# Kernel optimization log

Measured on AMD Instinct MI355X. Metric: run time of the kernel, lower is better.

The kernel has to match this reference:

```python
import jax, jax.numpy as jnp
import numpy as np

MU = 1.0          # stability parameter
DT = 0.01         # Euler step
EPS = 1e-9        # matches E in the torch source
BOUND = float(np.pi / 2)  # hard_bounds = (-pi/2, pi/2)
N_NODES = 200_000
N_EDGES = 12_800_000  # avg degree 64


def setup_inputs() -> dict:
    key = jax.random.key(0)
    ks = jax.random.split(key, 9)
    n, ne = N_NODES, N_EDGES
    # distributions mirror the torch initialization
    x = jax.random.normal(ks[0], (n,), jnp.float32) * 0.1
    y = jax.random.normal(ks[1], (n,), jnp.float32) * 0.1
    w = (jax.random.uniform(ks[2], (n,), jnp.float32) * 2 - 1) * 4.0 + 2.0
    amplitudes = (jax.random.uniform(ks[3], (n,), jnp.float32) * 2 - 1) * 2.0 + 1.0
    phase = (jax.random.uniform(ks[4], (n,), jnp.float32) * 2 - 1) * np.pi
    ha = jax.random.normal(ks[5], (n,), jnp.float32) * 0.5
    b = jax.random.normal(ks[6], (n,), jnp.float32) * 0.1
    edge_src = jax.random.randint(ks[7], (ne,), 0, n, jnp.int32)
    edge_dst = jax.random.randint(ks[8], (ne,), 0, n, jnp.int32)
    return {"x": x, "y": y, "w": w, "amplitudes": amplitudes, "phase": phase,
            "ha": ha, "b": b, "edge_src": edge_src, "edge_dst": edge_dst}


def reference(x, y, w, amplitudes, phase, ha, b, edge_src, edge_dst):
    n = x.shape[0]
    # r^2 = x^2 + y^2 + E  (torch computes sqrt(..+E) then squares it)
    r2 = x * x + y * y + EPS
    dx = (MU - r2) * x - w * y
    dy = (MU - r2) * y + w * x
    # edge coupling: for edge (j=src -> i=dst):
    #   d*_i += ha_i * sin(theta_j - theta_i) * (*_j - *_i)
    theta = jnp.arctan2(y, x + EPS)                       # [n]
    coef = ha[edge_dst] * jnp.sin(theta[edge_src] - theta[edge_dst])  # [ne]
    cx = jax.ops.segment_sum(coef * (x[edge_src] - x[edge_dst]), edge_dst, num_segments=n)
    cy = jax.ops.segment_sum(coef * (y[edge_src] - y[edge_dst]), edge_dst, num_segments=n)
    # Euler step (x update is internal state; angles depend only on new y)
    y_new = y + (dy + cy) * DT
    x_new = x + (dx + cx) * DT
    angles = amplitudes * y_new + phase + b
    angles = jnp.clip(angles, -BOUND, BOUND)
    return angles
```

## Files before the change

### kernel.cpp

```cpp
#include <hip/hip_runtime.h>
#include <hip/hip_bf16.h>

#define MU_V    1.0f
#define DT_V    0.01f
#define EPS_V   1e-9f
#define BOUND_V 1.5707963267948966f

constexpr int NPB     = 1024;
constexpr int LOG_NPB = 10;
constexpr int NB_MAX  = 256;
constexpr int B1      = 512;
constexpr int EPT     = 16;
constexpr int EPB     = B1 * EPT;
constexpr int CAP     = 68608;
constexpr int RB      = 256;

static_assert(NB_MAX == 256, "block scan below assumes NB_MAX == 256 (4 waves)");

typedef unsigned uint4v __attribute__((ext_vector_type(4)));

__global__ void node_pre_kernel(const float* __restrict__ x_,
                                const float* __restrict__ y_,
                                const float* __restrict__ ha_,
                                float4* __restrict__ pack,
                                unsigned* __restrict__ zbuf,
                                int n, int nz) {
    int i = blockIdx.x * blockDim.x + threadIdx.x;
    if (i < nz) zbuf[i] = 0u;
    if (i >= n) return;
    float x = x_[i];
    float y = y_[i];
    float xe = x + EPS_V;
    float r2 = xe * xe + y * y;
    float s, c;
    if (r2 > 0.0f) {
        float rinv = rsqrtf(r2);
        s = y * rinv;
        c = xe * rinv;
    } else {
        s = 0.0f;
        c = 1.0f;
    }
    pack[i] = make_float4(s, c, y, ha_[i]);
}

__global__ __launch_bounds__(B1)
void bucket_scatter_kernel(const int* __restrict__ src,
                           const int* __restrict__ dst,
                           unsigned* __restrict__ cursors,
                           unsigned* __restrict__ buf,
                           int ne, int nb) {
    __shared__ unsigned cnt[NB_MAX];
    __shared__ unsigned gbase[NB_MAX];
    __shared__ unsigned lofs[NB_MAX];
    __shared__ unsigned loc[NB_MAX];
    __shared__ unsigned wsum[4];
    __shared__ unsigned ents[EPB];

    int tid = threadIdx.x;
    for (int i = tid; i < NB_MAX; i += B1) cnt[i] = 0u;
    __syncthreads();
    long long base = (long long)blockIdx.x * EPB;

    if (base + EPB <= ne) {
        int4 rs4[EPT / 4], rd4[EPT / 4];
        #pragma unroll
        for (int it = 0; it < EPT / 4; ++it) {
            long long e = base + ((long long)(it * B1 + tid)) * 4;
            rs4[it] = *(const int4*)(src + e);
            rd4[it] = *(const int4*)(dst + e);
        }
        const int* sv = (const int*)rs4;
        const int* dv = (const int*)rd4;
        #pragma unroll
        for (int k = 0; k < EPT; ++k)
            atomicAdd(&cnt[((unsigned)dv[k]) >> LOG_NPB], 1u);
        __syncthreads();

        unsigned myc = 0u, incl = 0u;
        if (tid < NB_MAX) {
            myc = cnt[tid];
            incl = myc;
            #pragma unroll
            for (int d = 1; d < 64; d <<= 1) {
                unsigned up = __shfl_up(incl, d);
                if ((tid & 63) >= d) incl += up;
            }
            if ((tid & 63) == 63) wsum[tid >> 6] = incl;
        }
        __syncthreads();
        if (tid < NB_MAX) {
            unsigned wp = 0u;
            int w = tid >> 6;
            #pragma unroll
            for (int k = 0; k < 3; ++k)
                if (k < w) wp += wsum[k];
            lofs[tid] = wp + incl - myc;
            gbase[tid] = myc ? atomicAdd(&cursors[tid], myc) : 0u;
            loc[tid] = 0u;
        }
        __syncthreads();

        #pragma unroll
        for (int k = 0; k < EPT; ++k) {
            unsigned d = (unsigned)dv[k];
            unsigned s = (unsigned)sv[k];
            unsigned b = d >> LOG_NPB;
            unsigned p = atomicAdd(&loc[b], 1u);
            ents[lofs[b] + p] = (s << LOG_NPB) | (d & (NPB - 1));
        }
        __syncthreads();

        int wave = tid >> 6;
        int lane = tid & 63;
        for (int b = wave; b < nb; b += (B1 / 64)) {
            unsigned c  = cnt[b];
            unsigned gb = gbase[b];
            unsigned lo = lofs[b];
            for (unsigned i = (unsigned)lane; i < c; i += 64u) {
                unsigned p = gb + i;
                if (p < (unsigned)CAP)
                    buf[(size_t)b * CAP + p] = ents[lo + i];
            }
        }
    } else {
        #pragma unroll
        for (int it = 0; it < EPT / 4; ++it) {
            long long e = base + ((long long)(it * B1 + tid)) * 4;
            if (e + 4 <= ne) {
                int4 d4 = *(const int4*)(dst + e);
                atomicAdd(&cnt[((unsigned)d4.x) >> LOG_NPB], 1u);
                atomicAdd(&cnt[((unsigned)d4.y) >> LOG_NPB], 1u);
                atomicAdd(&cnt[((unsigned)d4.z) >> LOG_NPB], 1u);
                atomicAdd(&cnt[((unsigned)d4.w) >> LOG_NPB], 1u);
            } else if (e < ne) {
                for (long long q = e; q < ne; ++q)
                    atomicAdd(&cnt[((unsigned)dst[q]) >> LOG_NPB], 1u);
            }
        }
        __syncthreads();
        for (int b = tid; b < nb; b += B1) {
            unsigned c = cnt[b];
            gbase[b] = c ? atomicAdd(&cursors[b], c) : 0u;
            loc[b] = 0u;
        }
        __syncthreads();
        #pragma unroll
        for (int it = 0; it < EPT / 4; ++it) {
            long long e = base + ((long long)(it * B1 + tid)) * 4;
            if (e + 4 <= ne) {
                int4 s4 = *(const int4*)(src + e);
                int4 d4 = *(const int4*)(dst + e);
                {
                    unsigned d = (unsigned)d4.x, s = (unsigned)s4.x, b = d >> LOG_NPB;
                    unsigned pos = gbase[b] + atomicAdd(&loc[b], 1u);
                    if (pos < (unsigned)CAP) buf[(size_t)b * CAP + pos] = (s << LOG_NPB) | (d & (NPB - 1));
                }
                {
                    unsigned d = (unsigned)d4.y, s = (unsigned)s4.y, b = d >> LOG_NPB;
                    unsigned pos = gbase[b] + atomicAdd(&loc[b], 1u);
                    if (pos < (unsigned)CAP) buf[(size_t)b * CAP + pos] = (s << LOG_NPB) | (d & (NPB - 1));
                }
                {
                    unsigned d = (unsigned)d4.z, s = (unsigned)s4.z, b = d >> LOG_NPB;
                    unsigned pos = gbase[b] + atomicAdd(&loc[b], 1u);
                    if (pos < (unsigned)CAP) buf[(size_t)b * CAP + pos] = (s << LOG_NPB) | (d & (NPB - 1));
                }
                {
                    unsigned d = (unsigned)d4.w, s = (unsigned)s4.w, b = d >> LOG_NPB;
                    unsigned pos = gbase[b] + atomicAdd(&loc[b], 1u);
                    if (pos < (unsigned)CAP) buf[(size_t)b * CAP + pos] = (s << LOG_NPB) | (d & (NPB - 1));
                }
            } else if (e < ne) {
                for (long long q = e; q < ne; ++q) {
                    unsigned d = (unsigned)dst[q], s = (unsigned)src[q], b = d >> LOG_NPB;
                    unsigned pos = gbase[b] + atomicAdd(&loc[b], 1u);
                    if (pos < (unsigned)CAP) buf[(size_t)b * CAP + pos] = (s << LOG_NPB) | (d & (NPB - 1));
                }
            }
        }
    }
}

__device__ __forceinline__ void reduce_entry(unsigned ent,
                                             const float4* __restrict__ pack,
                                             const float4* __restrict__ plocal,
                                             float* __restrict__ acc) {
    unsigned s  = ent >> LOG_NPB;
    unsigned dl = ent & (NPB - 1);
    float4 ps = pack[s];
    float4 pd = plocal[dl];
    float v = (pd.w * (ps.x * pd.y - ps.y * pd.x)) * (ps.z - pd.z);
    atomicAdd(&acc[dl], v);
}

__device__ __forceinline__ void reduce_proc(unsigned ent, float4 ps,
                                            const float4* __restrict__ plocal,
                                            float* __restrict__ acc) {
    unsigned dl = ent & (NPB - 1);
    float4 pd = plocal[dl];
    float v = (pd.w * (ps.x * pd.y - ps.y * pd.x)) * (ps.z - pd.z);
    atomicAdd(&acc[dl], v);
}

__global__ __launch_bounds__(RB)
void bucket_reduce_kernel(const unsigned* __restrict__ cursors,
                          const unsigned* __restrict__ buf,
                          const float4* __restrict__ pack,
                          float* __restrict__ partial, int n, int nsub) {
    __shared__ float4 plocal[NPB];
    __shared__ float  acc[NPB];
    int b   = blockIdx.x / nsub;
    int sub = blockIdx.x % nsub;
    int tid = threadIdx.x;
    int node0 = b << LOG_NPB;
    for (int k = tid; k < NPB; k += RB) {
        int d = node0 + k;
        plocal[k] = (d < n) ? pack[d] : make_float4(0.f, 0.f, 0.f, 0.f);
        acc[k] = 0.0f;
    }
    __syncthreads();
    unsigned count = cursors[b];
    if (count > (unsigned)CAP) count = (unsigned)CAP;
    unsigned chunk = (((count + nsub - 1) / nsub) + 7u) & ~7u;
    unsigned lo = (unsigned)sub * chunk;
    unsigned hi = lo + chunk;
    if (hi > count) hi = count;
    unsigned span = (hi > lo) ? (hi - lo) : 0u;
    unsigned vend = lo + (span & ~7u);
    const unsigned* mybuf = buf + (size_t)b * CAP;

    unsigned i = lo + (unsigned)tid * 8u;
    if (i < vend) {
        uint4v a4 = __builtin_nontemporal_load((const uint4v*)(mybuf + i));
        uint4v b4 = __builtin_nontemporal_load((const uint4v*)(mybuf + i + 4));
        while (true) {
            float4 g0 = pack[a4.x >> LOG_NPB];
            float4 g1 = pack[a4.y >> LOG_NPB];
            float4 g2 = pack[a4.z >> LOG_NPB];
            float4 g3 = pack[a4.w >> LOG_NPB];
            float4 g4 = pack[b4.x >> LOG_NPB];
            float4 g5 = pack[b4.y >> LOG_NPB];
            float4 g6 = pack[b4.z >> LOG_NPB];
            float4 g7 = pack[b4.w >> LOG_NPB];
            unsigned ni = i + (unsigned)RB * 8u;
            bool more = ni < vend;
            uint4v na4 = a4, nb4 = b4;
            if (more) {
                na4 = __builtin_nontemporal_load((const uint4v*)(mybuf + ni));
                nb4 = __builtin_nontemporal_load((const uint4v*)(mybuf + ni + 4));
            }
            reduce_proc(a4.x, g0, plocal, acc);
            reduce_proc(a4.y, g1, plocal, acc);
            reduce_proc(a4.z, g2, plocal, acc);
            reduce_proc(a4.w, g3, plocal, acc);
            reduce_proc(b4.x, g4, plocal, acc);
            reduce_proc(b4.y, g5, plocal, acc);
            reduce_proc(b4.z, g6, plocal, acc);
            reduce_proc(b4.w, g7, plocal, acc);
            if (!more) break;
            i = ni; a4 = na4; b4 = nb4;
        }
    }
    {
        unsigned idx = vend + (unsigned)tid;
        if (idx < hi)
            reduce_entry(mybuf[idx], pack, plocal, acc);
    }
    __syncthreads();
    float* myp = partial + ((size_t)b * nsub + sub) * NPB;
    for (int k = tid; k < NPB; k += RB)
        __builtin_nontemporal_store(acc[k], &myp[k]);
}

__device__ __forceinline__ void edge_one(int s, int d,
                                         const float4* __restrict__ pack,
                                         float* __restrict__ cy) {
    float4 ps = pack[s];
    float4 pd = pack[d];
    float v = (pd.w * (ps.x * pd.y - ps.y * pd.x)) * (ps.z - pd.z);
    atomicAdd(&cy[d], v);
}

__global__ void edge_kernel(const int* __restrict__ src,
                            const int* __restrict__ dst,
                            const float4* __restrict__ pack,
                            float* __restrict__ cy, int ne) {
    int t = blockIdx.x * blockDim.x + threadIdx.x;
    long long base = (long long)t * 4;
    if (base >= ne) return;
    if (base + 4 <= ne) {
        int4 s4 = *(const int4*)(src + base);
        int4 d4 = *(const int4*)(dst + base);
        edge_one(s4.x, d4.x, pack, cy);
        edge_one(s4.y, d4.y, pack, cy);
        edge_one(s4.z, d4.z, pack, cy);
        edge_one(s4.w, d4.w, pack, cy);
    } else {
        for (long long e = base; e < ne; ++e)
            edge_one(src[e], dst[e], pack, cy);
    }
}

__global__ void finalize_fast_kernel(const float* __restrict__ x_,
                                     const float* __restrict__ y_,
                                     const float* __restrict__ w_,
                                     const float* __restrict__ amp_,
                                     const float* __restrict__ ph_,
                                     const float* __restrict__ b_,
                                     const float* __restrict__ partial,
                                     float* __restrict__ out, int n, int nsub) {
    int i = blockIdx.x * blockDim.x + threadIdx.x;
    if (i >= n) return;
    int bk = i >> LOG_NPB;
    int dl = i & (NPB - 1);
    float cy = 0.0f;
    for (int s = 0; s < nsub; ++s)
        cy += partial[((size_t)bk * nsub + s) * NPB + dl];
    float x = x_[i];
    float y = y_[i];
    float w = w_[i];
    float r2 = x * x + y * y + EPS_V;
    float dy = (MU_V - r2) * y + w * x;
    float y_new = y + (dy + cy) * DT_V;
    float ang = amp_[i] * y_new + ph_[i] + b_[i];
    ang = fminf(fmaxf(ang, -BOUND_V), BOUND_V);
    out[i] = ang;
}

__global__ void finalize_kernel(const float* __restrict__ x_,
                                const float* __restrict__ y_,
                                const float* __restrict__ w_,
                                const float* __restrict__ amp_,
                                const float* __restrict__ ph_,
                                const float* __restrict__ b_,
                                const float* __restrict__ cy,
                                float* __restrict__ out, int n) {
    int i = blockIdx.x * blockDim.x + threadIdx.x;
    if (i >= n) return;
    float x = x_[i];
    float y = y_[i];
    float w = w_[i];
    float r2 = x * x + y * y + EPS_V;
    float dy = (MU_V - r2) * y + w * x;
    float y_new = y + (dy + cy[i]) * DT_V;
    float ang = amp_[i] * y_new + ph_[i] + b_[i];
    ang = fminf(fmaxf(ang, -BOUND_V), BOUND_V);
    out[i] = ang;
}

extern "C" void kernel_launch(void* const* d_in, const int* in_sizes, int n_in,
                              void* d_out, int out_size, void* d_ws, size_t ws_size,
                              hipStream_t stream) {
    const float* x_   = (const float*)d_in[0];
    const float* y_   = (const float*)d_in[1];
    const float* w_   = (const float*)d_in[2];
    const float* amp_ = (const float*)d_in[3];
    const float* ph_  = (const float*)d_in[4];
    const float* ha_  = (const float*)d_in[5];
    const float* b_   = (const float*)d_in[6];
    const int* edge_src = (const int*)d_in[7];
    const int* edge_dst = (const int*)d_in[8];
    float* out = (float*)d_out;

    int n  = in_sizes[0];
    int ne = in_sizes[7];
    int nb = (n + NPB - 1) >> LOG_NPB;

    auto align256 = [](size_t v) { return (v + 255) & ~(size_t)255; };
    size_t off_pack    = 0;
    size_t off_cursors = align256(off_pack + (size_t)n * 16);
    size_t off_partial = align256(off_cursors + (size_t)nb * 4);

    int nsub = 0;
    size_t off_buf = 0;
    for (int cand : {16, 12, 8, 4, 2, 1}) {
        size_t ob = align256(off_partial + (size_t)nb * cand * NPB * 4);
        if (ob + (size_t)nb * CAP * 4 <= ws_size) { nsub = cand; off_buf = ob; break; }
    }

    float4*   pack    = (float4*)((char*)d_ws + off_pack);
    unsigned* cursors = (unsigned*)((char*)d_ws + off_cursors);
    float*    cy      = (float*)((char*)d_ws + off_cursors);
    float*    partial = (float*)((char*)d_ws + off_partial);
    unsigned* buf     = (unsigned*)((char*)d_ws + off_buf);

    bool fast = (nsub > 0) && (nb <= NB_MAX) &&
                ((long long)n <= (1LL << (31 - LOG_NPB)));

    const int B = 256;
    if (fast) {
        node_pre_kernel<<<(n + B - 1) / B, B, 0, stream>>>(
            x_, y_, ha_, pack, cursors, n, nb);
        int blocks1 = (ne + EPB - 1) / EPB;
        bucket_scatter_kernel<<<blocks1, B1, 0, stream>>>(
            edge_src, edge_dst, cursors, buf, ne, nb);
        bucket_reduce_kernel<<<nb * nsub, RB, 0, stream>>>(
            cursors, buf, pack, partial, n, nsub);
        finalize_fast_kernel<<<(n + B - 1) / B, B, 0, stream>>>(
            x_, y_, w_, amp_, ph_, b_, partial, out, n, nsub);
    } else {
        node_pre_kernel<<<(n + B - 1) / B, B, 0, stream>>>(
            x_, y_, ha_, pack, (unsigned*)cy, n, n);
        int ngroups = (ne + 3) / 4;
        edge_kernel<<<(ngroups + B - 1) / B, B, 0, stream>>>(
            edge_src, edge_dst, pack, cy, ne);
        finalize_kernel<<<(n + B - 1) / B, B, 0, stream>>>(
            x_, y_, w_, amp_, ph_, b_, cy, out, n);
    }
}
```

Baseline: 261.7 us.

## Fuse node precompute into scatter and finalize into reduce via last-block ticket

Folds the node trig/pack precompute into the bucket scatter kernel and the final Euler/clip step into the bucket reduce kernel. The last sub-block per bucket is picked with an atomic ticket and threadfence, so four launches become two plus a memset. It also narrows the scatter write-out groups from 64 to 16 lanes and drops the software-pipelined prefetch in the reduce loop. The aim is to cut launch and small-kernel overhead, at the cost of extra fence/atomic work and possibly less latency hiding in the reduce loop.

```diff
diff --git a/kernel.cpp b/kernel.cpp
--- a/kernel.cpp
+++ b/kernel.cpp
@@ -16,6 +16,7 @@
 constexpr int RB      = 256;
 
 static_assert(NB_MAX == 256, "block scan below assumes NB_MAX == 256 (4 waves)");
+static_assert((CAP & 7) == 0, "CAP must be a multiple of 8 for vectored reads");
 
 typedef unsigned uint4v __attribute__((ext_vector_type(4)));
 
@@ -45,11 +46,15 @@
 }
 
 __global__ __launch_bounds__(B1)
-void bucket_scatter_kernel(const int* __restrict__ src,
+void bucket_scatter_kernel(const float* __restrict__ x_,
+                           const float* __restrict__ y_,
+                           const float* __restrict__ ha_,
+                           float4* __restrict__ pack,
+                           const int* __restrict__ src,
                            const int* __restrict__ dst,
                            unsigned* __restrict__ cursors,
                            unsigned* __restrict__ buf,
-                           int ne, int nb) {
+                           int ne, int nb, int n) {
     __shared__ unsigned cnt[NB_MAX];
     __shared__ unsigned gbase[NB_MAX];
     __shared__ unsigned lofs[NB_MAX];
@@ -58,6 +63,29 @@
     __shared__ unsigned ents[EPB];
 
     int tid = threadIdx.x;
+
+    {
+        int ns = (n + (int)gridDim.x - 1) / (int)gridDim.x;
+        int i0 = (int)blockIdx.x * ns;
+        int i1 = i0 + ns; if (i1 > n) i1 = n;
+        for (int i = i0 + tid; i < i1; i += B1) {
+            float x = x_[i];
+            float y = y_[i];
+            float xe = x + EPS_V;
+            float r2 = xe * xe + y * y;
+            float s, c;
+            if (r2 > 0.0f) {
+                float rinv = rsqrtf(r2);
+                s = y * rinv;
+                c = xe * rinv;
+            } else {
+                s = 0.0f;
+                c = 1.0f;
+            }
+            pack[i] = make_float4(s, c, y, ha_[i]);
+        }
+    }
+
     for (int i = tid; i < NB_MAX; i += B1) cnt[i] = 0u;
     __syncthreads();
     long long base = (long long)blockIdx.x * EPB;
@@ -111,13 +139,13 @@
         }
         __syncthreads();
 
-        int wave = tid >> 6;
-        int lane = tid & 63;
-        for (int b = wave; b < nb; b += (B1 / 64)) {
+        int grp = tid >> 4;
+        int l16 = tid & 15;
+        for (int b = grp; b < nb; b += (B1 / 16)) {
             unsigned c  = cnt[b];
             unsigned gb = gbase[b];
             unsigned lo = lofs[b];
-            for (unsigned i = (unsigned)lane; i < c; i += 64u) {
+            for (unsigned i = (unsigned)l16; i < c; i += 16u) {
                 unsigned p = gb + i;
                 if (p < (unsigned)CAP)
                     buf[(size_t)b * CAP + p] = ents[lo + i];
@@ -204,12 +232,22 @@
 }
 
 __global__ __launch_bounds__(RB)
-void bucket_reduce_kernel(const unsigned* __restrict__ cursors,
-                          const unsigned* __restrict__ buf,
-                          const float4* __restrict__ pack,
-                          float* __restrict__ partial, int n, int nsub) {
+void bucket_reduce_fin_kernel(const unsigned* __restrict__ cursors,
+                              unsigned* __restrict__ done,
+                              const unsigned* __restrict__ buf,
+                              const float4* __restrict__ pack,
+                              float* __restrict__ partial,
+                              const float* __restrict__ x_,
+                              const float* __restrict__ y_,
+                              const float* __restrict__ w_,
+                              const float* __restrict__ amp_,
+                              const float* __restrict__ ph_,
+                              const float* __restrict__ b_,
+                              float* __restrict__ out,
+                              int n, int nsub) {
     __shared__ float4 plocal[NPB];
     __shared__ float  acc[NPB];
+    __shared__ unsigned ticket_s;
     int b   = blockIdx.x / nsub;
     int sub = blockIdx.x % nsub;
     int tid = threadIdx.x;
@@ -230,37 +268,25 @@
     unsigned vend = lo + (span & ~7u);
     const unsigned* mybuf = buf + (size_t)b * CAP;
 
-    unsigned i = lo + (unsigned)tid * 8u;
-    if (i < vend) {
+    for (unsigned i = lo + (unsigned)tid * 8u; i < vend; i += (unsigned)RB * 8u) {
         uint4v a4 = __builtin_nontemporal_load((const uint4v*)(mybuf + i));
         uint4v b4 = __builtin_nontemporal_load((const uint4v*)(mybuf + i + 4));
-        while (true) {
-            float4 g0 = pack[a4.x >> LOG_NPB];
-            float4 g1 = pack[a4.y >> LOG_NPB];
-            float4 g2 = pack[a4.z >> LOG_NPB];
-            float4 g3 = pack[a4.w >> LOG_NPB];
-            float4 g4 = pack[b4.x >> LOG_NPB];
-            float4 g5 = pack[b4.y >> LOG_NPB];
-            float4 g6 = pack[b4.z >> LOG_NPB];
-            float4 g7 = pack[b4.w >> LOG_NPB];
-            unsigned ni = i + (unsigned)RB * 8u;
-            bool more = ni < vend;
-            uint4v na4 = a4, nb4 = b4;
-            if (more) {
-                na4 = __builtin_nontemporal_load((const uint4v*)(mybuf + ni));
-                nb4 = __builtin_nontemporal_load((const uint4v*)(mybuf + ni + 4));
-            }
-            reduce_proc(a4.x, g0, plocal, acc);
-            reduce_proc(a4.y, g1, plocal, acc);
-            reduce_proc(a4.z, g2, plocal, acc);
-            reduce_proc(a4.w, g3, plocal, acc);
-            reduce_proc(b4.x, g4, plocal, acc);
-            reduce_proc(b4.y, g5, plocal, acc);
-            reduce_proc(b4.z, g6, plocal, acc);
-            reduce_proc(b4.w, g7, plocal, acc);
-            if (!more) break;
-            i = ni; a4 = na4; b4 = nb4;
-        }
+        float4 g0 = pack[a4.x >> LOG_NPB];
+        float4 g1 = pack[a4.y >> LOG_NPB];
+        float4 g2 = pack[a4.z >> LOG_NPB];
+        float4 g3 = pack[a4.w >> LOG_NPB];
+        float4 g4 = pack[b4.x >> LOG_NPB];
+        float4 g5 = pack[b4.y >> LOG_NPB];
+        float4 g6 = pack[b4.z >> LOG_NPB];
+        float4 g7 = pack[b4.w >> LOG_NPB];
+        reduce_proc(a4.x, g0, plocal, acc);
+        reduce_proc(a4.y, g1, plocal, acc);
+        reduce_proc(a4.z, g2, plocal, acc);
+        reduce_proc(a4.w, g3, plocal, acc);
+        reduce_proc(b4.x, g4, plocal, acc);
+        reduce_proc(b4.y, g5, plocal, acc);
+        reduce_proc(b4.z, g6, plocal, acc);
+        reduce_proc(b4.w, g7, plocal, acc);
     }
     {
         unsigned idx = vend + (unsigned)tid;
@@ -268,9 +294,35 @@
             reduce_entry(mybuf[idx], pack, plocal, acc);
     }
     __syncthreads();
+
     float* myp = partial + ((size_t)b * nsub + sub) * NPB;
-    for (int k = tid; k < NPB; k += RB)
-        __builtin_nontemporal_store(acc[k], &myp[k]);
+    for (int k = tid; k < NPB; k += RB) myp[k] = acc[k];
+
+    __threadfence();
+    __syncthreads();
+    if (tid == 0) ticket_s = atomicAdd(&done[b], 1u);
+    __syncthreads();
+    if (ticket_s != (unsigned)(nsub - 1)) return;
+
+    __threadfence();
+    for (int k = tid; k < NPB; k += RB) {
+        int i = node0 + k;
+        if (i >= n) continue;
+        float cy = acc[k];
+        for (int s2 = 0; s2 < nsub; ++s2) {
+            if (s2 == sub) continue;
+            cy += partial[((size_t)b * nsub + s2) * NPB + k];
+        }
+        float x = x_[i];
+        float y = y_[i];
+        float w = w_[i];
+        float r2 = x * x + y * y + EPS_V;
+        float dy = (MU_V - r2) * y + w * x;
+        float y_new = y + (dy + cy) * DT_V;
+        float ang = amp_[i] * y_new + ph_[i] + b_[i];
+        ang = fminf(fmaxf(ang, -BOUND_V), BOUND_V);
+        out[i] = ang;
+    }
 }
 
 __device__ __forceinline__ void edge_one(int s, int d,
@@ -300,32 +352,6 @@
         for (long long e = base; e < ne; ++e)
             edge_one(src[e], dst[e], pack, cy);
     }
-}
-
-__global__ void finalize_fast_kernel(const float* __restrict__ x_,
-                                     const float* __restrict__ y_,
-                                     const float* __restrict__ w_,
-                                     const float* __restrict__ amp_,
-                                     const float* __restrict__ ph_,
-                                     const float* __restrict__ b_,
-                                     const float* __restrict__ partial,
-                                     float* __restrict__ out, int n, int nsub) {
-    int i = blockIdx.x * blockDim.x + threadIdx.x;
-    if (i >= n) return;
-    int bk = i >> LOG_NPB;
-    int dl = i & (NPB - 1);
-    float cy = 0.0f;
-    for (int s = 0; s < nsub; ++s)
-        cy += partial[((size_t)bk * nsub + s) * NPB + dl];
-    float x = x_[i];
-    float y = y_[i];
-    float w = w_[i];
-    float r2 = x * x + y * y + EPS_V;
-    float dy = (MU_V - r2) * y + w * x;
-    float y_new = y + (dy + cy) * DT_V;
-    float ang = amp_[i] * y_new + ph_[i] + b_[i];
-    ang = fminf(fmaxf(ang, -BOUND_V), BOUND_V);
-    out[i] = ang;
 }
 
 __global__ void finalize_kernel(const float* __restrict__ x_,
@@ -370,7 +396,8 @@
     auto align256 = [](size_t v) { return (v + 255) & ~(size_t)255; };
     size_t off_pack    = 0;
     size_t off_cursors = align256(off_pack + (size_t)n * 16);
-    size_t off_partial = align256(off_cursors + (size_t)nb * 4);
+    size_t off_done    = off_cursors + (size_t)nb * 4;
+    size_t off_partial = align256(off_done + (size_t)nb * 4);
 
     int nsub = 0;
     size_t off_buf = 0;
@@ -381,6 +408,7 @@
 
     float4*   pack    = (float4*)((char*)d_ws + off_pack);
     unsigned* cursors = (unsigned*)((char*)d_ws + off_cursors);
+    unsigned* done    = (unsigned*)((char*)d_ws + off_done);
     float*    cy      = (float*)((char*)d_ws + off_cursors);
     float*    partial = (float*)((char*)d_ws + off_partial);
     unsigned* buf     = (unsigned*)((char*)d_ws + off_buf);
@@ -390,15 +418,13 @@
 
     const int B = 256;
     if (fast) {
-        node_pre_kernel<<<(n + B - 1) / B, B, 0, stream>>>(
-            x_, y_, ha_, pack, cursors, n, nb);
+        hipMemsetAsync((char*)d_ws + off_cursors, 0, (size_t)nb * 8, stream);
         int blocks1 = (ne + EPB - 1) / EPB;
         bucket_scatter_kernel<<<blocks1, B1, 0, stream>>>(
-            edge_src, edge_dst, cursors, buf, ne, nb);
-        bucket_reduce_kernel<<<nb * nsub, RB, 0, stream>>>(
-            cursors, buf, pack, partial, n, nsub);
-        finalize_fast_kernel<<<(n + B - 1) / B, B, 0, stream>>>(
-            x_, y_, w_, amp_, ph_, b_, partial, out, n, nsub);
+            x_, y_, ha_, pack, edge_src, edge_dst, cursors, buf, ne, nb, n);
+        bucket_reduce_fin_kernel<<<nb * nsub, RB, 0, stream>>>(
+            cursors, done, buf, pack, partial,
+            x_, y_, w_, amp_, ph_, b_, out, n, nsub);
     } else {
         node_pre_kernel<<<(n + B - 1) / B, B, 0, stream>>>(
             x_, y_, ha_, pack, (unsigned*)cy, n, n);
```

After: 752.2 us. +187.5%, slower.
